# Optimization experiments

Measured on AMD Instinct MI355X. Metric: run time of the kernel, lower is better.

Reference implementation:

```python
import jax, jax.numpy as jnp
import numpy as np

N_EMBED = 2048
N_HEAD = 16
HEAD_DIM = N_EMBED // N_HEAD
ROPE_BASE = 500000


def _rope_cos_sin(T, dim, base):
    # torchtune RotaryPositionalEmbeddings: interleaved pairs
    inv_freq = 1.0 / (base ** (jnp.arange(0, dim, 2, dtype=jnp.float32) / dim))  # [dim/2]
    pos = jnp.arange(T, dtype=jnp.float32)
    ang = pos[:, None] * inv_freq[None, :]  # [T, dim/2]
    return jnp.cos(ang), jnp.sin(ang)


def _apply_rope(x, cos, sin):
    # x: [B, T, H, D]; cos/sin: [T, D/2] -> broadcast [1, T, 1, D/2]
    c = cos[None, :, None, :]
    s = sin[None, :, None, :]
    x1 = x[..., 0::2]
    x2 = x[..., 1::2]
    r1 = x1 * c - x2 * s
    r2 = x2 * c + x1 * s
    return jnp.stack([r1, r2], axis=-1).reshape(x.shape)


def setup_inputs() -> dict:
    key = jax.random.key(0)
    k1, k2, k3 = jax.random.split(key, 3)
    B, T, C = 4, 2048, N_EMBED
    x = jax.random.normal(k1, (B, T, C), dtype=jnp.float32)
    Wqkv = jax.random.normal(k2, (C, 3 * C), dtype=jnp.float32) * 0.02
    Wproj = jax.random.normal(k3, (C, C), dtype=jnp.float32) * 0.02
    return {"x": x, "Wqkv": Wqkv, "Wproj": Wproj}


def reference(x, Wqkv, Wproj):
    B, T, C = x.shape
    H, D = N_HEAD, HEAD_DIM
    qkv = x @ Wqkv  # [B, T, 3C]
    q, k, v = jnp.split(qkv, 3, axis=2)
    q = q.reshape(B, T, H, D)
    k = k.reshape(B, T, H, D)
    v = v.reshape(B, T, H, D)
    cos, sin = _rope_cos_sin(T, D, ROPE_BASE)
    q = _apply_rope(q, cos, sin)
    k = _apply_rope(k, cos, sin)
    scale = 1.0 / jnp.sqrt(jnp.float32(D))
    # causal SDPA: scores [B, H, T, T]
    scores = jnp.einsum('bqhd,bkhd->bhqk', q, k) * scale
    mask = jnp.tril(jnp.ones((T, T), dtype=bool))
    scores = jnp.where(mask[None, None, :, :], scores, jnp.float32(-1e30))
    attn = jax.nn.softmax(scores, axis=-1)
    y = jnp.einsum('bhqk,bkhd->bqhd', attn, v).reshape(B, T, C)
    return y @ Wproj
```

## Files before the change

### kernel.cpp

```cpp
#include <hip/hip_runtime.h>
#include <math.h>

#define NB 4
#define TT 2048
#define CC 2048
#define HH 16
#define DD 128
#define N3 6144
#define MM 8192
#define BH 64

typedef short bf8 __attribute__((ext_vector_type(8)));
typedef float f32x4 __attribute__((ext_vector_type(4)));
typedef unsigned short u16x8 __attribute__((ext_vector_type(8)));
typedef unsigned short u16;

constexpr float SCALE_QK  = 0.08838834764831843f;
constexpr float NEG_ALPHA = -0.20503692777194262f;

__device__ __forceinline__ u16 f2bf(float x) {
    unsigned int u = __float_as_uint(x);
    u += 0x7fffu + ((u >> 16) & 1u);
    return (u16)(u >> 16);
}
__device__ __forceinline__ float bf2f(u16 h) { return __uint_as_float(((unsigned int)h) << 16); }

__device__ __forceinline__ void gl_lds16(const u16* g, u16* l) {
    __builtin_amdgcn_global_load_lds(reinterpret_cast<const unsigned int*>(g),
                                     reinterpret_cast<unsigned int*>(l), 16, 0, 0);
}
__device__ __forceinline__ f32x4 MFMA(bf8 a, bf8 b, f32x4 c) {
    return __builtin_amdgcn_mfma_f32_16x16x32_bf16(a, b, c, 0, 0, 0);
}

#define BAR()    __builtin_amdgcn_s_barrier()
#define SCHED0() __builtin_amdgcn_sched_barrier(0)
#define WAIT_LGKM0() do { asm volatile("s_waitcnt lgkmcnt(0)" ::: "memory"); SCHED0(); } while (0)
#define WAIT_VM8()   do { asm volatile("s_waitcnt vmcnt(8)"   ::: "memory"); SCHED0(); } while (0)
#define WAIT_VM4()   do { asm volatile("s_waitcnt vmcnt(4)"   ::: "memory"); SCHED0(); } while (0)
#define WAIT_VM0()   do { asm volatile("s_waitcnt vmcnt(0)"   ::: "memory"); SCHED0(); } while (0)

__global__ void rope_tab_k(float* __restrict__ tab) {
    int t = blockIdx.x, p = threadIdx.x;
    float inv = expf((float)p * NEG_ALPHA);
    float s, c;
    sincosf((float)t * inv, &s, &c);
    tab[(t * 64 + p) * 2]     = c;
    tab[(t * 64 + p) * 2 + 1] = s;
}

__global__ __launch_bounds__(256) void split_x_k(const float* __restrict__ X,
                                                 u16* __restrict__ H, u16* __restrict__ L) {
    size_t base = ((size_t)blockIdx.x * 256 + threadIdx.x) * 16;
    #pragma unroll
    for (int g = 0; g < 2; ++g) {
        u16x8 hv, lv;
        #pragma unroll
        for (int j = 0; j < 8; j += 4) {
            float4 a = *(const float4*)(X + base + g * 8 + j);
            float xs[4] = {a.x, a.y, a.z, a.w};
            #pragma unroll
            for (int q = 0; q < 4; ++q) {
                u16 h = f2bf(xs[q]);
                hv[j + q] = h;
                lv[j + q] = f2bf(xs[q] - bf2f(h));
            }
        }
        *(u16x8*)&H[base + g * 8] = hv;
        *(u16x8*)&L[base + g * 8] = lv;
    }
}

__global__ __launch_bounds__(256) void splitT_h(const float* __restrict__ W,
                                                u16* __restrict__ OH,
                                                int Kd, int Nd) {
    __shared__ float tile[64][68];
    int k0 = blockIdx.x * 64, n0 = blockIdx.y * 64;
    {
        int r = threadIdx.x >> 2, cg = threadIdx.x & 3;
        const float* src = W + (size_t)(k0 + r) * Nd + n0 + cg * 16;
        #pragma unroll
        for (int j = 0; j < 4; ++j)
            *(float4*)&tile[r][cg * 16 + j * 4] = *(const float4*)(src + j * 4);
    }
    __syncthreads();
    int nl = threadIdx.x >> 2, kg = threadIdx.x & 3;
    u16x8 hv[2];
    #pragma unroll
    for (int j = 0; j < 16; ++j)
        hv[j >> 3][j & 7] = f2bf(tile[kg * 16 + j][nl]);
    size_t off = (size_t)(n0 + nl) * Kd + k0 + kg * 16;
    *(u16x8*)&OH[off]     = hv[0];
    *(u16x8*)&OH[off + 8] = hv[1];
}

template<int MODE>
__global__ __launch_bounds__(512, 2) void gemm8p(
    const u16* __restrict__ Ahp, const u16* __restrict__ Alp,
    const u16* __restrict__ Bhp,
    u16* __restrict__ Qh, u16* __restrict__ Ql,
    u16* __restrict__ Kbo, u16* __restrict__ Vto,
    const float* __restrict__ tab, float* __restrict__ Out)
{
    __shared__ u16 SM[66048];

    const int tid = threadIdx.x;
    const int w = tid >> 6, ln = tid & 63;
    const int lo4 = ln & 15, hi4 = ln >> 4;
    const int wr = w >> 2, wc = w & 3;
    const int m0 = blockIdx.x * 256, n0 = blockIdx.y * 256;
    const int NKT = 64;

    f32x4 acc[8][4];
    #pragma unroll
    for (int i = 0; i < 8; ++i)
        #pragma unroll
        for (int j = 0; j < 4; ++j) acc[i][j] = (f32x4){0.f, 0.f, 0.f, 0.f};

    auto stage = [&](int s) {
        if (s >= 4 * NKT) return;
        const int tau = s >> 2, j = s & 3;
        const int c2 = tau & 1, op = j >> 1, hf = j & 1;
        const int tdiv = tau >> 5, tmod = tau & 31;
        const u16* plane;
        int row0;
        if (op == 0) { plane = tdiv ? Alp : Ahp; row0 = m0 + hf * 128; }
        else         { plane = Bhp;              row0 = n0 + hf * 128; }
        u16* dst = SM + (op ? 32768 : 0) + (c2 * 2 + hf) * 8192;
        #pragma unroll
        for (int i = 0; i < 2; ++i) {
            int L = i * 8192 + tid * 16;
            int r = L >> 7;
            int c = (L >> 4) & 7;
            int cs = c ^ (r & 7);
            gl_lds16(plane + (size_t)(row0 + r) * 2048 + tmod * 64 + cs * 8,
                     dst + (L >> 1));
        }
    };

    #pragma unroll
    for (int s = 0; s < 6; ++s) stage(s);
    WAIT_VM4();
    BAR();

    bf8 a03[4][2], a47[4][2], b01[2][2], b23[2][2];
    const int brow0 = (wc & 1) * 64;

    for (int t = 0; t < NKT; ++t) {
        const int c2 = t & 1;
        const u16* Ab = SM + (c2 * 2 + wr) * 8192;
        const u16* Bb = SM + 32768 + (c2 * 2 + (wc >> 1)) * 8192;

        #pragma unroll
        for (int mf = 0; mf < 4; ++mf) {
            int rr = mf * 16 + lo4, s7 = rr & 7;
            a03[mf][0] = *(const bf8*)&Ab[rr * 64 + ((hi4 ^ s7)) * 8];
            a03[mf][1] = *(const bf8*)&Ab[rr * 64 + (((4 + hi4) ^ s7)) * 8];
        }
        #pragma unroll
        for (int nf = 0; nf < 2; ++nf) {
            int rr = brow0 + nf * 16 + lo4, s7 = rr & 7;
            b01[nf][0] = *(const bf8*)&Bb[rr * 64 + ((hi4 ^ s7)) * 8];
            b01[nf][1] = *(const bf8*)&Bb[rr * 64 + (((4 + hi4) ^ s7)) * 8];
        }
        stage(4 * t + 6);
        BAR(); WAIT_LGKM0();
        __builtin_amdgcn_s_setprio(1);
        #pragma unroll
        for (int mf = 0; mf < 4; ++mf)
            #pragma unroll
            for (int nf = 0; nf < 2; ++nf) {
                acc[mf][nf] = MFMA(a03[mf][0], b01[nf][0], acc[mf][nf]);
                acc[mf][nf] = MFMA(a03[mf][1], b01[nf][1], acc[mf][nf]);
            }
        __builtin_amdgcn_s_setprio(0);
        BAR();

        #pragma unroll
        for (int mf = 0; mf < 4; ++mf) {
            int rr = 64 + mf * 16 + lo4, s7 = rr & 7;
            a47[mf][0] = *(const bf8*)&Ab[rr * 64 + ((hi4 ^ s7)) * 8];
            a47[mf][1] = *(const bf8*)&Ab[rr * 64 + (((4 + hi4) ^ s7)) * 8];
        }
        stage(4 * t + 7);
        BAR(); WAIT_LGKM0();
        __builtin_amdgcn_s_setprio(1);
        #pragma unroll
        for (int mf = 0; mf < 4; ++mf)
            #pragma unroll
            for (int nf = 0; nf < 2; ++nf) {
                acc[4 + mf][nf] = MFMA(a47[mf][0], b01[nf][0], acc[4 + mf][nf]);
                acc[4 + mf][nf] = MFMA(a47[mf][1], b01[nf][1], acc[4 + mf][nf]);
            }
        __builtin_amdgcn_s_setprio(0);
        BAR();

        #pragma unroll
        for (int nf = 0; nf < 2; ++nf) {
            int rr = brow0 + 32 + nf * 16 + lo4, s7 = rr & 7;
            b23[nf][0] = *(const bf8*)&Bb[rr * 64 + ((hi4 ^ s7)) * 8];
            b23[nf][1] = *(const bf8*)&Bb[rr * 64 + (((4 + hi4) ^ s7)) * 8];
        }
        stage(4 * t + 8);
        BAR(); WAIT_LGKM0();
        __builtin_amdgcn_s_setprio(1);
        #pragma unroll
        for (int mf = 0; mf < 4; ++mf)
            #pragma unroll
            for (int nf = 0; nf < 2; ++nf) {
                acc[mf][2 + nf] = MFMA(a03[mf][0], b23[nf][0], acc[mf][2 + nf]);
                acc[mf][2 + nf] = MFMA(a03[mf][1], b23[nf][1], acc[mf][2 + nf]);
            }
        __builtin_amdgcn_s_setprio(0);
        BAR();

        stage(4 * t + 9);
        BAR();
        __builtin_amdgcn_s_setprio(1);
        #pragma unroll
        for (int mf = 0; mf < 4; ++mf)
            #pragma unroll
            for (int nf = 0; nf < 2; ++nf) {
                acc[4 + mf][2 + nf] = MFMA(a47[mf][0], b23[nf][0], acc[4 + mf][2 + nf]);
                acc[4 + mf][2 + nf] = MFMA(a47[mf][1], b23[nf][1], acc[4 + mf][2 + nf]);
            }
        __builtin_amdgcn_s_setprio(0);
        if (t < NKT - 2)       { WAIT_VM4(); }
        else if (t == NKT - 2) { WAIT_VM0(); }
        BAR();
    }

    if (MODE == 1) {
        #pragma unroll
        for (int mf = 0; mf < 8; ++mf)
            #pragma unroll
            for (int r = 0; r < 4; ++r) {
                int m = m0 + wr * 128 + mf * 16 + hi4 * 4 + r;
                float* rowp = Out + (size_t)m * CC + n0 + wc * 64;
                #pragma unroll
                for (int nf = 0; nf < 4; ++nf)
                    rowp[nf * 16 + lo4] = acc[mf][nf][r];
            }
        return;
    }

    const int sec = n0 >> 11;
    const int hh0 = (n0 >> 7) & 15;
    if (sec < 2) {
        #pragma unroll
        for (int mf = 0; mf < 8; ++mf)
            #pragma unroll
            for (int r = 0; r < 4; ++r) {
                int m = m0 + wr * 128 + mf * 16 + hi4 * 4 + r;
                int t = m & 2047, b = m >> 11;
                #pragma unroll
                for (int nf = 0; nf < 4; ++nf) {
                    int nl = wc * 64 + nf * 16 + lo4;
                    int h = hh0 + (nl >> 7), d = nl & 127;
                    float v = acc[mf][nf][r];
                    float o = __shfl_xor(v, 1);
                    const float2 cs2 = *(const float2*)&tab[(((size_t)t << 6) + (d >> 1)) * 2];
                    float rv = (ln & 1) ? (v * cs2.x + o * cs2.y)
                                        : (v * cs2.x - o * cs2.y);
                    size_t off = (((size_t)(b * HH + h)) * TT + t) * DD + d;
                    if (sec == 0) {
                        rv *= SCALE_QK;
                        u16 hv = f2bf(rv);
                        Qh[off] = hv;
                        Ql[off] = f2bf(rv - bf2f(hv));
                    } else {
                        Kbo[off] = f2bf(rv);
                    }
                }
            }
    } else {
        BAR();
        #pragma unroll
        for (int mf = 0; mf < 8; ++mf)
            #pragma unroll
            for (int r = 0; r < 4; ++r) {
                int tl = wr * 128 + mf * 16 + hi4 * 4 + r;
                #pragma unroll
                for (int nf = 0; nf < 4; ++nf) {
                    int nl = wc * 64 + nf * 16 + lo4;
                    SM[tl * 258 + nl] = f2bf(acc[mf][nf][r]);
                }
            }
        BAR();
        int nl = tid >> 1, th = tid & 1;
        int head = hh0 + (nl >> 7), d = nl & 127;
        int b = m0 >> 11, t0 = m0 & 2047;
        size_t base = (((size_t)(b * HH + head)) * DD + d) * TT + t0 + th * 128;
        #pragma unroll
        for (int g = 0; g < 16; ++g) {
            u16x8 vv;
            #pragma unroll
            for (int j = 0; j < 8; ++j) vv[j] = SM[(th * 128 + g * 8 + j) * 258 + nl];
            *(u16x8*)&Vto[base + g * 8] = vv;
        }
    }
}

__global__ __launch_bounds__(256, 2) void attn128(
    const u16* __restrict__ Qhp, const u16* __restrict__ Qlp,
    const u16* __restrict__ Kb,  const u16* __restrict__ Vt,
    u16* __restrict__ Yh, u16* __restrict__ Yl)
{
    __shared__ u16 SM[40960];

    const int tid = threadIdx.x;
    const int w = tid >> 6, ln = tid & 63;
    const int lo4 = ln & 15, hi4 = ln >> 4;
    const int bx = blockIdx.x;
    const int qt = (bx & 1) ? (15 - (bx >> 1)) : (bx >> 1);
    const int bh = blockIdx.y;
    const int q0 = qt * 128;
    const int last = 2 * qt + 1;

    const size_t qoff = ((size_t)bh * TT + q0) * DD;
    #pragma unroll
    for (int i = 0; i < 8; ++i) {
        int L = i * 4096 + tid * 16;
        int r = L >> 8, c = (L >> 4) & 15;
        int cs = c ^ (r & 7);
        gl_lds16(Qhp + qoff + r * DD + cs * 8, &SM[L >> 1]);
        gl_lds16(Qlp + qoff + r * DD + cs * 8, &SM[16384 + (L >> 1)]);
    }
    WAIT_VM0();
    BAR();
    bf8 qh[2][4], ql[2][4];
    #pragma unroll
    for (int mf = 0; mf < 2; ++mf) {
        int rq = w * 32 + mf * 16 + lo4, s7 = rq & 7;
        #pragma unroll
        for (int ks = 0; ks < 4; ++ks) {
            int ch = (ks * 4 + hi4) ^ s7;
            qh[mf][ks] = *(const bf8*)&SM[rq * 128 + ch * 8];
            ql[mf][ks] = *(const bf8*)&SM[16384 + rq * 128 + ch * 8];
        }
    }
    WAIT_LGKM0();
    BAR();

    auto stageKV = [&](int kt2, int buf) {
        const size_t koff = ((size_t)bh * TT + kt2 * 64) * DD;
        u16* kd = &SM[buf * 8192];
        #pragma unroll
        for (int i = 0; i < 4; ++i) {
            int L = i * 4096 + tid * 16;
            int r = L >> 8, c = (L >> 4) & 15, cs = c ^ (r & 7);
            gl_lds16(Kb + koff + r * DD + cs * 8, kd + (L >> 1));
        }
        const size_t voff = (size_t)bh * DD * TT + (size_t)kt2 * 64;
        u16* vd = &SM[16384 + buf * 8192];
        #pragma unroll
        for (int i = 0; i < 4; ++i) {
            int L = i * 4096 + tid * 16;
            int r = L >> 7, c = (L >> 4) & 7, cs = c ^ (r & 7);
            gl_lds16(Vt + voff + (size_t)r * TT + cs * 8, vd + (L >> 1));
        }
    };
    stageKV(0, 0);

    f32x4 O[2][8];
    #pragma unroll
    for (int mf = 0; mf < 2; ++mf)
        #pragma unroll
        for (int i = 0; i < 8; ++i) O[mf][i] = (f32x4){0.f, 0.f, 0.f, 0.f};
    float m_r[2][4], l_r[2][4];
    #pragma unroll
    for (int mf = 0; mf < 2; ++mf)
        #pragma unroll
        for (int r = 0; r < 4; ++r) { m_r[mf][r] = -1e30f; l_r[mf][r] = 0.f; }

    for (int kt = 0; kt <= last; ++kt) {
        const int cur = kt & 1;
        if (kt < last) { stageKV(kt + 1, cur ^ 1); WAIT_VM8(); }
        else           { WAIT_VM0(); }
        BAR();
        const u16* Kcur = &SM[cur * 8192];
        const u16* Vcur = &SM[16384 + cur * 8192];

        f32x4 sf[2][4];
        #pragma unroll
        for (int nf = 0; nf < 4; ++nf) {
            f32x4 s0 = (f32x4){0.f, 0.f, 0.f, 0.f};
            f32x4 s1 = (f32x4){0.f, 0.f, 0.f, 0.f};
            int kr = nf * 16 + lo4, s7 = kr & 7;
            #pragma unroll
            for (int ks = 0; ks < 4; ++ks) {
                bf8 bb = *(const bf8*)&Kcur[kr * 128 + ((ks * 4 + hi4) ^ s7) * 8];
                s0 = MFMA(qh[0][ks], bb, s0);
                s0 = MFMA(ql[0][ks], bb, s0);
                s1 = MFMA(qh[1][ks], bb, s1);
                s1 = MFMA(ql[1][ks], bb, s1);
            }
            sf[0][nf] = s0; sf[1][nf] = s1;
        }
        if (kt >= 2 * qt) {
            #pragma unroll
            for (int mf = 0; mf < 2; ++mf)
                #pragma unroll
                for (int nf = 0; nf < 4; ++nf)
                    #pragma unroll
                    for (int r = 0; r < 4; ++r) {
                        int kg = kt * 64 + nf * 16 + lo4;
                        int qg = q0 + w * 32 + mf * 16 + hi4 * 4 + r;
                        if (kg > qg) sf[mf][nf][r] = -1e30f;
                    }
        }

        #pragma unroll
        for (int mf = 0; mf < 2; ++mf) {
            float mx[4];
            #pragma unroll
            for (int r = 0; r < 4; ++r) {
                float m2 = fmaxf(fmaxf(sf[mf][0][r], sf[mf][1][r]),
                                 fmaxf(sf[mf][2][r], sf[mf][3][r]));
                m2 = fmaxf(m2, __shfl_xor(m2, 1));
                m2 = fmaxf(m2, __shfl_xor(m2, 2));
                m2 = fmaxf(m2, __shfl_xor(m2, 4));
                m2 = fmaxf(m2, __shfl_xor(m2, 8));
                mx[r] = m2;
            }
            float al[4] = {1.f, 1.f, 1.f, 1.f};
            bool grow = (mx[0] > m_r[mf][0]) || (mx[1] > m_r[mf][1]) ||
                        (mx[2] > m_r[mf][2]) || (mx[3] > m_r[mf][3]);
            if (__any(grow)) {
                #pragma unroll
                for (int r = 0; r < 4; ++r) {
                    float mn = fmaxf(m_r[mf][r], mx[r]);
                    al[r] = __expf(m_r[mf][r] - mn);
                    m_r[mf][r] = mn;
                }
                #pragma unroll
                for (int nf2 = 0; nf2 < 8; ++nf2)
                    #pragma unroll
                    for (int r = 0; r < 4; ++r) O[mf][nf2][r] *= al[r];
            }
            #pragma unroll
            for (int r = 0; r < 4; ++r) {
                float rs = 0.f;
                #pragma unroll
                for (int nf = 0; nf < 4; ++nf) {
                    float p = __expf(sf[mf][nf][r] - m_r[mf][r]);
                    sf[mf][nf][r] = p;
                    rs += p;
                }
                rs += __shfl_xor(rs, 1);
                rs += __shfl_xor(rs, 2);
                rs += __shfl_xor(rs, 4);
                rs += __shfl_xor(rs, 8);
                l_r[mf][r] = l_r[mf][r] * al[r] + rs;
            }
        }

        u16* pw = &SM[32768 + w * 2048];
        #pragma unroll
        for (int mf = 0; mf < 2; ++mf)
            #pragma unroll
            for (int r = 0; r < 4; ++r) {
                int row = mf * 16 + hi4 * 4 + r;
                int sw = (row & 7) << 3;
                #pragma unroll
                for (int nf = 0; nf < 4; ++nf)
                    pw[row * 64 + ((nf * 16 + lo4) ^ sw)] = f2bf(sf[mf][nf][r]);
            }
        bf8 pa[2][2];
        #pragma unroll
        for (int mf = 0; mf < 2; ++mf) {
            int rp = mf * 16 + lo4, s3 = rp & 7;
            pa[mf][0] = *(const bf8*)&pw[rp * 64 + ((hi4 ^ s3) * 8)];
            pa[mf][1] = *(const bf8*)&pw[rp * 64 + (((4 + hi4) ^ s3) * 8)];
        }
        #pragma unroll
        for (int nf2 = 0; nf2 < 8; ++nf2) {
            int vr = nf2 * 16 + lo4, s7 = vr & 7;
            #pragma unroll
            for (int ks = 0; ks < 2; ++ks) {
                bf8 vb = *(const bf8*)&Vcur[vr * 64 + ((ks * 4 + hi4) ^ s7) * 8];
                O[0][nf2] = MFMA(pa[0][ks], vb, O[0][nf2]);
                O[1][nf2] = MFMA(pa[1][ks], vb, O[1][nf2]);
            }
        }
        BAR();
    }

    const int b = bh >> 4, h = bh & 15;
    #pragma unroll
    for (int mf = 0; mf < 2; ++mf)
        #pragma unroll
        for (int r = 0; r < 4; ++r) {
            float inv = 1.0f / l_r[mf][r];
            int t = q0 + w * 32 + mf * 16 + hi4 * 4 + r;
            size_t rowo = ((size_t)(b * TT + t)) * CC + h * DD;
            #pragma unroll
            for (int nf2 = 0; nf2 < 8; ++nf2) {
                float val = O[mf][nf2][r] * inv;
                u16 hv = f2bf(val);
                Yh[rowo + nf2 * 16 + lo4] = hv;
                Yl[rowo + nf2 * 16 + lo4] = f2bf(val - bf2f(hv));
            }
        }
}

extern "C" void kernel_launch(void* const* d_in, const int* in_sizes, int n_in,
                              void* d_out, int out_size, void* d_ws, size_t ws_size,
                              hipStream_t stream)
{
    const float* X     = (const float*)d_in[0];
    const float* Wqkv  = (const float*)d_in[1];
    const float* Wproj = (const float*)d_in[2];

    char* W = (char*)d_ws;
    float* tab = (float*)W;
    u16* Wqh = (u16*)(W + (1u << 20));
    u16* Wph = Wqh + 12582912;
    u16* Xh  = Wph + 4194304;
    u16* Xl  = Xh + 16777216;
    u16* Kb  = Xl + 16777216;
    u16* Vt  = Kb + 16777216;

    u16* Qh = (u16*)d_out;
    u16* Ql = Qh + 16777216;

    u16* Yh = Xh;
    u16* Yl = Xl;

    rope_tab_k<<<dim3(2048), 64, 0, stream>>>(tab);
    split_x_k<<<dim3(4096), 256, 0, stream>>>(X, Xh, Xl);
    splitT_h<<<dim3(32, 96), 256, 0, stream>>>(Wqkv, Wqh, 2048, 6144);
    splitT_h<<<dim3(32, 32), 256, 0, stream>>>(Wproj, Wph, 2048, 2048);

    gemm8p<0><<<dim3(32, 24), 512, 0, stream>>>(Xh, Xl, Wqh,
                                                Qh, Ql, Kb, Vt, tab, nullptr);
    attn128<<<dim3(16, 64), 256, 0, stream>>>(Qh, Ql, Kb, Vt, Yh, Yl);
    gemm8p<1><<<dim3(32, 8), 512, 0, stream>>>(Yh, Yl, Wph,
                                               nullptr, nullptr, nullptr, nullptr,
                                               nullptr, (float*)d_out);
}
```

Measured before the change: 1.017 ms.

## Precompute staging addresses, fold log2e into Q scale, prioritize attention MFMAs

```diff
diff --git a/kernel.cpp b/kernel.cpp
--- a/kernel.cpp
+++ b/kernel.cpp
@@ -16,6 +16,7 @@
 typedef unsigned short u16;
 
 constexpr float SCALE_QK  = 0.08838834764831843f;
+constexpr float SCALE_Q2  = 0.08838834764831843f * 1.44269504088896f;
 constexpr float NEG_ALPHA = -0.20503692777194262f;
 
 __device__ __forceinline__ u16 f2bf(float x) {
@@ -95,20 +96,21 @@
 }
 
 template<int MODE>
-__global__ __launch_bounds__(512, 2) void gemm8p(
+__device__ __forceinline__ void g16_body(
     const u16* __restrict__ Ahp, const u16* __restrict__ Alp,
     const u16* __restrict__ Bhp,
     u16* __restrict__ Qh, u16* __restrict__ Ql,
     u16* __restrict__ Kbo, u16* __restrict__ Vto,
-    const float* __restrict__ tab, float* __restrict__ Out)
+    const float* __restrict__ tab, float* __restrict__ Out,
+    int bx, int by)
 {
-    __shared__ u16 SM[66048];
+    __shared__ __align__(16) u16 SM[66048];
 
     const int tid = threadIdx.x;
     const int w = tid >> 6, ln = tid & 63;
     const int lo4 = ln & 15, hi4 = ln >> 4;
     const int wr = w >> 2, wc = w & 3;
-    const int m0 = blockIdx.x * 256, n0 = blockIdx.y * 256;
+    const int m0 = bx * 256, n0 = by * 256;
     const int NKT = 64;
 
     f32x4 acc[8][4];
@@ -117,29 +119,49 @@
         #pragma unroll
         for (int j = 0; j < 4; ++j) acc[i][j] = (f32x4){0.f, 0.f, 0.f, 0.f};
 
-    auto stage = [&](int s) {
-        if (s >= 4 * NKT) return;
-        const int tau = s >> 2, j = s & 3;
-        const int c2 = tau & 1, op = j >> 1, hf = j & 1;
-        const int tdiv = tau >> 5, tmod = tau & 31;
-        const u16* plane;
-        int row0;
-        if (op == 0) { plane = tdiv ? Alp : Ahp; row0 = m0 + hf * 128; }
-        else         { plane = Bhp;              row0 = n0 + hf * 128; }
-        u16* dst = SM + (op ? 32768 : 0) + (c2 * 2 + hf) * 8192;
-        #pragma unroll
-        for (int i = 0; i < 2; ++i) {
-            int L = i * 8192 + tid * 16;
-            int r = L >> 7;
-            int c = (L >> 4) & 7;
-            int cs = c ^ (r & 7);
-            gl_lds16(plane + (size_t)(row0 + r) * 2048 + tmod * 64 + cs * 8,
-                     dst + (L >> 1));
-        }
+    const int r0  = tid >> 3;
+    const int cs0 = (tid & 7) ^ (r0 & 7);
+    const size_t sA0 = (size_t)(m0 + r0) * 2048 + cs0 * 8;
+    const size_t sA1 = sA0 + (size_t)128 * 2048;
+    const size_t sB0 = (size_t)(n0 + r0) * 2048 + cs0 * 8;
+    const size_t sB1 = sB0 + (size_t)128 * 2048;
+    const size_t sStep = (size_t)64 * 2048;
+    u16* const dA0 = SM + tid * 8;
+    u16* const dB0 = SM + 32768 + tid * 8;
+
+    auto STAGE_A0 = [&](int tau) {
+        if (tau >= NKT) return;
+        const u16* pl = (tau < 32) ? Ahp : Alp;
+        const size_t o = sA0 + (size_t)(tau & 31) * 64;
+        u16* d = dA0 + (tau & 1) * 16384;
+        gl_lds16(pl + o, d);
+        gl_lds16(pl + o + sStep, d + 4096);
     };
-
-    #pragma unroll
-    for (int s = 0; s < 6; ++s) stage(s);
+    auto STAGE_A1 = [&](int tau) {
+        if (tau >= NKT) return;
+        const u16* pl = (tau < 32) ? Ahp : Alp;
+        const size_t o = sA1 + (size_t)(tau & 31) * 64;
+        u16* d = dA0 + (tau & 1) * 16384 + 8192;
+        gl_lds16(pl + o, d);
+        gl_lds16(pl + o + sStep, d + 4096);
+    };
+    auto STAGE_B0 = [&](int tau) {
+        if (tau >= NKT) return;
+        const size_t o = sB0 + (size_t)(tau & 31) * 64;
+        u16* d = dB0 + (tau & 1) * 16384;
+        gl_lds16(Bhp + o, d);
+        gl_lds16(Bhp + o + sStep, d + 4096);
+    };
+    auto STAGE_B1 = [&](int tau) {
+        if (tau >= NKT) return;
+        const size_t o = sB1 + (size_t)(tau & 31) * 64;
+        u16* d = dB0 + (tau & 1) * 16384 + 8192;
+        gl_lds16(Bhp + o, d);
+        gl_lds16(Bhp + o + sStep, d + 4096);
+    };
+
+    STAGE_A0(0); STAGE_A1(0); STAGE_B0(0); STAGE_B1(0);
+    STAGE_A0(1); STAGE_A1(1);
     WAIT_VM4();
     BAR();
 
@@ -163,7 +185,7 @@
             b01[nf][0] = *(const bf8*)&Bb[rr * 64 + ((hi4 ^ s7)) * 8];
             b01[nf][1] = *(const bf8*)&Bb[rr * 64 + (((4 + hi4) ^ s7)) * 8];
         }
-        stage(4 * t + 6);
+        STAGE_B0(t + 1);
         BAR(); WAIT_LGKM0();
         __builtin_amdgcn_s_setprio(1);
         #pragma unroll
@@ -182,7 +204,7 @@
             a47[mf][0] = *(const bf8*)&Ab[rr * 64 + ((hi4 ^ s7)) * 8];
             a47[mf][1] = *(const bf8*)&Ab[rr * 64 + (((4 + hi4) ^ s7)) * 8];
         }
-        stage(4 * t + 7);
+        STAGE_B1(t + 1);
         BAR(); WAIT_LGKM0();
         __builtin_amdgcn_s_setprio(1);
         #pragma unroll
@@ -201,7 +223,7 @@
             b23[nf][0] = *(const bf8*)&Bb[rr * 64 + ((hi4 ^ s7)) * 8];
             b23[nf][1] = *(const bf8*)&Bb[rr * 64 + (((4 + hi4) ^ s7)) * 8];
         }
-        stage(4 * t + 8);
+        STAGE_A0(t + 2);
         BAR(); WAIT_LGKM0();
         __builtin_amdgcn_s_setprio(1);
         #pragma unroll
@@ -214,7 +236,7 @@
         __builtin_amdgcn_s_setprio(0);
         BAR();
 
-        stage(4 * t + 9);
+        STAGE_A1(t + 2);
         BAR();
         __builtin_amdgcn_s_setprio(1);
         #pragma unroll
@@ -264,7 +286,7 @@
                                         : (v * cs2.x - o * cs2.y);
                     size_t off = (((size_t)(b * HH + h)) * TT + t) * DD + d;
                     if (sec == 0) {
-                        rv *= SCALE_QK;
+                        rv *= SCALE_Q2;
                         u16 hv = f2bf(rv);
                         Qh[off] = hv;
                         Ql[off] = f2bf(rv - bf2f(hv));
@@ -301,12 +323,30 @@
     }
 }
 
+__global__ __launch_bounds__(512, 2) void qkv_g16(
+    const u16* __restrict__ Ahp, const u16* __restrict__ Alp,
+    const u16* __restrict__ Bhp,
+    u16* __restrict__ Qh, u16* __restrict__ Ql,
+    u16* __restrict__ Kbo, u16* __restrict__ Vto,
+    const float* __restrict__ tab)
+{
+    g16_body<0>(Ahp, Alp, Bhp, Qh, Ql, Kbo, Vto, tab, nullptr,
+                blockIdx.x, blockIdx.y);
+}
+__global__ __launch_bounds__(512, 2) void proj_g16(
+    const u16* __restrict__ Ahp, const u16* __restrict__ Alp,
+    const u16* __restrict__ Bhp, float* __restrict__ Out)
+{
+    g16_body<1>(Ahp, Alp, Bhp, nullptr, nullptr, nullptr, nullptr,
+                nullptr, Out, blockIdx.x, blockIdx.y);
+}
+
 __global__ __launch_bounds__(256, 2) void attn128(
     const u16* __restrict__ Qhp, const u16* __restrict__ Qlp,
     const u16* __restrict__ Kb,  const u16* __restrict__ Vt,
     u16* __restrict__ Yh, u16* __restrict__ Yl)
 {
-    __shared__ u16 SM[40960];
+    __shared__ __align__(16) u16 SM[40960];
 
     const int tid = threadIdx.x;
     const int w = tid >> 6, ln = tid & 63;
@@ -317,14 +357,16 @@
     const int q0 = qt * 128;
     const int last = 2 * qt + 1;
 
-    const size_t qoff = ((size_t)bh * TT + q0) * DD;
-    #pragma unroll
-    for (int i = 0; i < 8; ++i) {
-        int L = i * 4096 + tid * 16;
-        int r = L >> 8, c = (L >> 4) & 15;
-        int cs = c ^ (r & 7);
-        gl_lds16(Qhp + qoff + r * DD + cs * 8, &SM[L >> 1]);
-        gl_lds16(Qlp + qoff + r * DD + cs * 8, &SM[16384 + (L >> 1)]);
+    {
+        const int qSrc0 = ((tid >> 4) * 128) + (((tid & 15) ^ ((tid >> 4) & 7)) * 8);
+        const u16* qs = Qhp + ((size_t)bh * TT + q0) * DD + qSrc0;
+        const u16* qls = Qlp + ((size_t)bh * TT + q0) * DD + qSrc0;
+        u16* qd = SM + tid * 8;
+        #pragma unroll
+        for (int i = 0; i < 8; ++i) {
+            gl_lds16(qs + i * 2048, qd + i * 2048);
+            gl_lds16(qls + i * 2048, qd + 16384 + i * 2048);
+        }
     }
     WAIT_VM0();
     BAR();
@@ -342,23 +384,21 @@
     WAIT_LGKM0();
     BAR();
 
+    const size_t kBase = (size_t)bh * TT * DD;
+    const size_t vBase = (size_t)bh * DD * TT;
+    const int kSrc0 = ((tid >> 4) * 128) + (((tid & 15) ^ ((tid >> 4) & 7)) * 8);
+    const int vSrc0 = ((tid >> 3) * 2048) + (((tid & 7) ^ ((tid >> 3) & 7)) * 8);
     auto stageKV = [&](int kt2, int buf) {
-        const size_t koff = ((size_t)bh * TT + kt2 * 64) * DD;
-        u16* kd = &SM[buf * 8192];
-        #pragma unroll
-        for (int i = 0; i < 4; ++i) {
-            int L = i * 4096 + tid * 16;
-            int r = L >> 8, c = (L >> 4) & 15, cs = c ^ (r & 7);
-            gl_lds16(Kb + koff + r * DD + cs * 8, kd + (L >> 1));
-        }
-        const size_t voff = (size_t)bh * DD * TT + (size_t)kt2 * 64;
-        u16* vd = &SM[16384 + buf * 8192];
-        #pragma unroll
-        for (int i = 0; i < 4; ++i) {
-            int L = i * 4096 + tid * 16;
-            int r = L >> 7, c = (L >> 4) & 7, cs = c ^ (r & 7);
-            gl_lds16(Vt + voff + (size_t)r * TT + cs * 8, vd + (L >> 1));
-        }
+        const u16* ks = Kb + kBase + kt2 * 8192 + kSrc0;
+        u16* kd = SM + buf * 8192 + tid * 8;
+        #pragma unroll
+        for (int i = 0; i < 4; ++i)
+            gl_lds16(ks + i * 2048, kd + i * 2048);
+        const u16* vs = Vt + vBase + kt2 * 64 + vSrc0;
+        u16* vd = SM + 16384 + buf * 8192 + tid * 8;
+        #pragma unroll
+        for (int i = 0; i < 4; ++i)
+            gl_lds16(vs + i * 65536, vd + i * 2048);
     };
     stageKV(0, 0);
 
@@ -382,6 +422,7 @@
         const u16* Vcur = &SM[16384 + cur * 8192];
 
         f32x4 sf[2][4];
+        __builtin_amdgcn_s_setprio(1);
         #pragma unroll
         for (int nf = 0; nf < 4; ++nf) {
             f32x4 s0 = (f32x4){0.f, 0.f, 0.f, 0.f};
@@ -397,6 +438,7 @@
             }
             sf[0][nf] = s0; sf[1][nf] = s1;
         }
+        __builtin_amdgcn_s_setprio(0);
         if (kt >= 2 * qt) {
             #pragma unroll
             for (int mf = 0; mf < 2; ++mf)
@@ -430,7 +472,7 @@
                 #pragma unroll
                 for (int r = 0; r < 4; ++r) {
                     float mn = fmaxf(m_r[mf][r], mx[r]);
-                    al[r] = __expf(m_r[mf][r] - mn);
+                    al[r] = exp2f(m_r[mf][r] - mn);
                     m_r[mf][r] = mn;
                 }
                 #pragma unroll
@@ -443,7 +485,7 @@
                 float rs = 0.f;
                 #pragma unroll
                 for (int nf = 0; nf < 4; ++nf) {
-                    float p = __expf(sf[mf][nf][r] - m_r[mf][r]);
+                    float p = exp2f(sf[mf][nf][r] - m_r[mf][r]);
                     sf[mf][nf][r] = p;
                     rs += p;
                 }
@@ -473,6 +515,7 @@
             pa[mf][0] = *(const bf8*)&pw[rp * 64 + ((hi4 ^ s3) * 8)];
             pa[mf][1] = *(const bf8*)&pw[rp * 64 + (((4 + hi4) ^ s3) * 8)];
         }
+        __builtin_amdgcn_s_setprio(1);
         #pragma unroll
         for (int nf2 = 0; nf2 < 8; ++nf2) {
             int vr = nf2 * 16 + lo4, s7 = vr & 7;
@@ -483,6 +526,7 @@
                 O[1][nf2] = MFMA(pa[1][ks], vb, O[1][nf2]);
             }
         }
+        __builtin_amdgcn_s_setprio(0);
         BAR();
     }
 
@@ -532,10 +576,7 @@
     splitT_h<<<dim3(32, 96), 256, 0, stream>>>(Wqkv, Wqh, 2048, 6144);
     splitT_h<<<dim3(32, 32), 256, 0, stream>>>(Wproj, Wph, 2048, 2048);
 
-    gemm8p<0><<<dim3(32, 24), 512, 0, stream>>>(Xh, Xl, Wqh,
-                                                Qh, Ql, Kb, Vt, tab, nullptr);
+    qkv_g16<<<dim3(32, 24), 512, 0, stream>>>(Xh, Xl, Wqh, Qh, Ql, Kb, Vt, tab);
     attn128<<<dim3(16, 64), 256, 0, stream>>>(Qh, Ql, Kb, Vt, Yh, Yl);
-    gemm8p<1><<<dim3(32, 8), 512, 0, stream>>>(Yh, Yl, Wph,
-                                               nullptr, nullptr, nullptr, nullptr,
-                                               nullptr, (float*)d_out);
-}
+    proj_g16<<<dim3(32, 8), 512, 0, stream>>>(Yh, Yl, Wph, (float*)d_out);
+}
```

Measured after the change: 1.002 ms. Within noise of the previous version (-1.5%).
